# Performance work log

Measured on AMD Instinct MI355X. Metric: run time of the kernel, lower is better.

The kernel has to match this reference:

```python
import jax, jax.numpy as jnp
import numpy as np

B = 128      # args.batch_size
E = 256      # args.num_embed
M = 64       # per-sample positions per embedding channel
S = 3        # number of scales == conv kernel width
C = 5        # args.classes
SCALES = [4, 8, 16]
EPS = 1e-5


def _rnn_last(x, wih, whh, bih, bhh):
    """Elman RNN with input/hidden size 1 over x:(N,T,1); returns last hidden (N,)."""
    xT = jnp.transpose(x[:, :, 0])  # (T, N)
    def step(h, xt):
        h = jnp.tanh(xt * wih + bih + h * whh + bhh)
        return h, None
    h0 = jnp.zeros((x.shape[0],), x.dtype)
    hT, _ = jax.lax.scan(step, h0, xT)
    return hT


def setup_inputs() -> dict:
    key = jax.random.key(0)
    ks = jax.random.split(key, 20)
    N = B * M * E
    inp = {}
    for i, T in enumerate(SCALES):
        inp[f"a{i}"] = jax.random.normal(ks[i], (N, T, 1), dtype=jnp.float32)
    sc = 0.5
    inp["rnn1_wih"] = sc * jax.random.normal(ks[3], (S,), dtype=jnp.float32)
    inp["rnn1_whh"] = sc * jax.random.normal(ks[4], (S,), dtype=jnp.float32)
    inp["rnn1_bih"] = sc * jax.random.normal(ks[5], (S,), dtype=jnp.float32)
    inp["rnn1_bhh"] = sc * jax.random.normal(ks[6], (S,), dtype=jnp.float32)
    inp["conv_w"] = sc * jax.random.normal(ks[7], (S,), dtype=jnp.float32)
    inp["conv_b"] = sc * jax.random.normal(ks[8], (1,), dtype=jnp.float32)
    inp["rnn2_wih"] = sc * jax.random.normal(ks[9], (1,), dtype=jnp.float32)
    inp["rnn2_whh"] = sc * jax.random.normal(ks[10], (1,), dtype=jnp.float32)
    inp["rnn2_bih"] = sc * jax.random.normal(ks[11], (1,), dtype=jnp.float32)
    inp["rnn2_bhh"] = sc * jax.random.normal(ks[12], (1,), dtype=jnp.float32)
    inp["norm_gamma"] = jnp.ones((E,), dtype=jnp.float32)
    inp["norm_beta"] = jnp.zeros((E,), dtype=jnp.float32)
    inp["fnn_w"] = jax.random.normal(ks[13], (C, E), dtype=jnp.float32) / C
    inp["fnn_b"] = jnp.zeros((C,), dtype=jnp.float32)
    return inp


def reference(a0, a1, a2, rnn1_wih, rnn1_whh, rnn1_bih, rnn1_bhh,
              conv_w, conv_b, rnn2_wih, rnn2_whh, rnn2_bih, rnn2_bhh,
              norm_gamma, norm_beta, fnn_w, fnn_b):
    # per-scale scalar RNNs; keep last hidden state, reshape to (B, M, E, 1)
    rst = []
    for i, a in enumerate((a0, a1, a2)):
        h = _rnn_last(a, rnn1_wih[i], rnn1_whh[i], rnn1_bih[i], rnn1_bhh[i])
        rst.append(h.reshape(B, M, E, 1))
    c = jnp.concatenate(rst, axis=-1)          # (B, M, E, S)
    cp = jnp.transpose(c, (0, 2, 1, 3))        # (B, E, M, S)
    # Conv2d(1,1,(1,3)) over (M,S) with S==kernel width -> single output column
    fusion = jnp.einsum('bems,s->bem', cp, conv_w) + conv_b[0]  # (B, E, M)
    # second scalar RNN over the M axis for each (b, e) lane
    seq2 = fusion.reshape(B * E, M, 1)
    h2 = _rnn_last(seq2, rnn2_wih[0], rnn2_whh[0], rnn2_bih[0], rnn2_bhh[0])
    feat = h2.reshape(B, E)
    # BatchNorm1d (training-mode batch statistics, biased variance)
    mean = feat.mean(axis=0)
    var = feat.var(axis=0)
    xn = (feat - mean) / jnp.sqrt(var + EPS) * norm_gamma + norm_beta
    logits = jax.nn.relu(xn) @ fnn_w.T + fnn_b  # (B, C)
    return jax.nn.softmax(logits, axis=1)
```

## Files before the change

kernel.cpp:

```cpp
#include <hip/hip_runtime.h>
#include <math.h>

#define Bb 128
#define Ee 256
#define Mm 64
#define Cc 5
#define NTOT (Bb*Mm*Ee)
#define BE  (Bb*Ee)
#define EPS 1e-5f
#define L2E2 2.8853900817779268f

#if __has_builtin(__builtin_amdgcn_exp2f)
#define EXP2(x) __builtin_amdgcn_exp2f(x)
#else
#define EXP2(x) exp2f(x)
#endif
#define RCP(x) __builtin_amdgcn_rcpf(x)

__device__ __forceinline__ float tanh_step(float x, float w, float b, float u, float h) {
    float t = __builtin_fmaf(x, w, b);
    t = __builtin_fmaf(h, u, t);
    float r = RCP(EXP2(t) + 1.0f);
    return __builtin_fmaf(-2.0f, r, 1.0f);
}

__global__ __launch_bounds__(256) void k_rnn1(
    const float* __restrict__ a0, const float* __restrict__ a1,
    const float* __restrict__ a2,
    const float* __restrict__ wih, const float* __restrict__ whh,
    const float* __restrict__ bih, const float* __restrict__ bhh,
    const float* __restrict__ cw,  const float* __restrict__ cb,
    float* __restrict__ fusion)
{
    int t = blockIdx.x * blockDim.x + threadIdx.x;

    float w0 = wih[0] * L2E2, w1 = wih[1] * L2E2, w2 = wih[2] * L2E2;
    float u0 = whh[0] * L2E2, u1 = whh[1] * L2E2, u2 = whh[2] * L2E2;
    float b0 = (bih[0] + bhh[0]) * L2E2;
    float b1 = (bih[1] + bhh[1]) * L2E2;
    float b2 = (bih[2] + bhh[2]) * L2E2;
    float c0 = cw[0], c1 = cw[1], c2 = cw[2], cbias = cb[0];

    #pragma unroll
    for (int s = 0; s < 2; ++s) {
        int n = t + s * (NTOT / 2);

        float4 x0 = ((const float4*)a0)[n];
        float h0 = tanh_step(x0.x, w0, b0, u0, 0.0f);
        h0 = tanh_step(x0.y, w0, b0, u0, h0);
        h0 = tanh_step(x0.z, w0, b0, u0, h0);
        h0 = tanh_step(x0.w, w0, b0, u0, h0);

        float4 y0 = ((const float4*)a1)[2*n + 0];
        float4 y1 = ((const float4*)a1)[2*n + 1];
        float h1 = tanh_step(y0.x, w1, b1, u1, 0.0f);
        h1 = tanh_step(y0.y, w1, b1, u1, h1);
        h1 = tanh_step(y0.z, w1, b1, u1, h1);
        h1 = tanh_step(y0.w, w1, b1, u1, h1);
        h1 = tanh_step(y1.x, w1, b1, u1, h1);
        h1 = tanh_step(y1.y, w1, b1, u1, h1);
        h1 = tanh_step(y1.z, w1, b1, u1, h1);
        h1 = tanh_step(y1.w, w1, b1, u1, h1);

        float h2 = 0.0f;
        #pragma unroll
        for (int q = 0; q < 4; ++q) {
            float4 z = ((const float4*)a2)[4*n + q];
            h2 = tanh_step(z.x, w2, b2, u2, h2);
            h2 = tanh_step(z.y, w2, b2, u2, h2);
            h2 = tanh_step(z.z, w2, b2, u2, h2);
            h2 = tanh_step(z.w, w2, b2, u2, h2);
        }

        float f = h0 * c0 + h1 * c1 + h2 * c2 + cbias;

        int e = n & (Ee - 1);
        int m = (n >> 8) & (Mm - 1);
        int b = n >> 14;
        fusion[(m << 15) + (b << 8) + e] = f;
    }
}

__global__ __launch_bounds__(256) void k_rnn2(
    const float* __restrict__ fusion,
    const float* __restrict__ w, const float* __restrict__ u,
    const float* __restrict__ bi, const float* __restrict__ bh,
    float* __restrict__ feat)
{
    int j = blockIdx.x * blockDim.x + threadIdx.x;
    float wv = w[0] * L2E2, uv = u[0] * L2E2, bb = (bi[0] + bh[0]) * L2E2;
    float h = 0.0f;
    #pragma unroll 8
    for (int m = 0; m < Mm; ++m) {
        float x = fusion[m * BE + j];
        h = tanh_step(x, wv, bb, uv, h);
    }
    feat[j] = h;
}

__global__ __launch_bounds__(256) void k_stats(
    const float* __restrict__ feat,
    const float* __restrict__ gamma, const float* __restrict__ beta,
    float* __restrict__ scale, float* __restrict__ shift)
{
    int e = threadIdx.x;
    float s = 0.0f, s2 = 0.0f;
    for (int b = 0; b < Bb; ++b) {
        float v = feat[b * Ee + e];
        s  += v;
        s2 += v * v;
    }
    float mean = s * (1.0f / Bb);
    float var  = s2 * (1.0f / Bb) - mean * mean;
    float a = gamma[e] * rsqrtf(var + EPS);
    scale[e] = a;
    shift[e] = beta[e] - mean * a;
}

__global__ __launch_bounds__(256) void k_head(
    const float* __restrict__ feat,
    const float* __restrict__ scale, const float* __restrict__ shift,
    const float* __restrict__ fw, const float* __restrict__ fb,
    float* __restrict__ out)
{
    int b = blockIdx.x;
    int e = threadIdx.x;

    float v = feat[b * Ee + e] * scale[e] + shift[e];
    v = fmaxf(v, 0.0f);

    float p[Cc];
    #pragma unroll
    for (int c = 0; c < Cc; ++c) p[c] = v * fw[c * Ee + e];

    #pragma unroll
    for (int off = 32; off > 0; off >>= 1) {
        #pragma unroll
        for (int c = 0; c < Cc; ++c) p[c] += __shfl_down(p[c], off);
    }

    __shared__ float lds[4][Cc];
    int wave = e >> 6, lane = e & 63;
    if (lane == 0) {
        #pragma unroll
        for (int c = 0; c < Cc; ++c) lds[wave][c] = p[c];
    }
    __syncthreads();

    if (e == 0) {
        float lg[Cc];
        #pragma unroll
        for (int c = 0; c < Cc; ++c)
            lg[c] = lds[0][c] + lds[1][c] + lds[2][c] + lds[3][c] + fb[c];
        float mx = lg[0];
        #pragma unroll
        for (int c = 1; c < Cc; ++c) mx = fmaxf(mx, lg[c]);
        float se = 0.0f;
        #pragma unroll
        for (int c = 0; c < Cc; ++c) { lg[c] = EXP2((lg[c] - mx) * 1.4426950408889634f); se += lg[c]; }
        float inv = RCP(se);
        #pragma unroll
        for (int c = 0; c < Cc; ++c) out[b * Cc + c] = lg[c] * inv;
    }
}

extern "C" void kernel_launch(void* const* d_in, const int* in_sizes, int n_in,
                              void* d_out, int out_size, void* d_ws, size_t ws_size,
                              hipStream_t stream) {
    const float* a0       = (const float*)d_in[0];
    const float* a1       = (const float*)d_in[1];
    const float* a2       = (const float*)d_in[2];
    const float* rnn1_wih = (const float*)d_in[3];
    const float* rnn1_whh = (const float*)d_in[4];
    const float* rnn1_bih = (const float*)d_in[5];
    const float* rnn1_bhh = (const float*)d_in[6];
    const float* conv_w   = (const float*)d_in[7];
    const float* conv_b   = (const float*)d_in[8];
    const float* rnn2_wih = (const float*)d_in[9];
    const float* rnn2_whh = (const float*)d_in[10];
    const float* rnn2_bih = (const float*)d_in[11];
    const float* rnn2_bhh = (const float*)d_in[12];
    const float* gamma    = (const float*)d_in[13];
    const float* beta     = (const float*)d_in[14];
    const float* fnn_w    = (const float*)d_in[15];
    const float* fnn_b    = (const float*)d_in[16];

    float* out = (float*)d_out;

    char* ws = (char*)d_ws;
    float* fusion = (float*)ws;
    float* feat   = (float*)(ws + (size_t)Mm * BE * 4);
    float* scale  = feat + BE;
    float* shift  = scale + Ee;

    k_rnn1<<<NTOT / 2 / 256, 256, 0, stream>>>(a0, a1, a2,
        rnn1_wih, rnn1_whh, rnn1_bih, rnn1_bhh, conv_w, conv_b, fusion);
    k_rnn2<<<BE / 256, 256, 0, stream>>>(fusion,
        rnn2_wih, rnn2_whh, rnn2_bih, rnn2_bhh, feat);
    k_stats<<<1, 256, 0, stream>>>(feat, gamma, beta, scale, shift);
    k_head<<<Bb, 256, 0, stream>>>(feat, scale, shift, fnn_w, fnn_b, out);
}
```

Baseline: 52.08 us.

## Coalesce rnn1 input loads via LDS transpose and fuse BN stats into head

```diff
diff --git a/kernel.cpp b/kernel.cpp
--- a/kernel.cpp
+++ b/kernel.cpp
@@ -32,7 +32,35 @@
     const float* __restrict__ cw,  const float* __restrict__ cb,
     float* __restrict__ fusion)
 {
-    int t = blockIdx.x * blockDim.x + threadIdx.x;
+    __shared__ float a1s[8 * 256];
+    __shared__ float a2s[16 * 257];
+
+    const int t   = threadIdx.x;
+    const int blk = blockIdx.x;
+    const int base = blk << 8;
+
+    float4 x0 = ((const float4*)a0)[base + t];
+
+    #pragma unroll
+    for (int r = 0; r < 2; ++r) {
+        int c = (r << 8) + t;
+        float4 v = ((const float4*)a1)[(size_t)(base << 1) + c];
+        int s = c >> 1, row = (c & 1) << 2;
+        a1s[(row + 0) * 256 + s] = v.x;
+        a1s[(row + 1) * 256 + s] = v.y;
+        a1s[(row + 2) * 256 + s] = v.z;
+        a1s[(row + 3) * 256 + s] = v.w;
+    }
+    #pragma unroll
+    for (int r = 0; r < 4; ++r) {
+        int c = (r << 8) + t;
+        float4 v = ((const float4*)a2)[(size_t)(base << 2) + c];
+        int s = c >> 2, row = (c & 3) << 2;
+        a2s[(row + 0) * 257 + s] = v.x;
+        a2s[(row + 1) * 257 + s] = v.y;
+        a2s[(row + 2) * 257 + s] = v.z;
+        a2s[(row + 3) * 257 + s] = v.w;
+    }
 
     float w0 = wih[0] * L2E2, w1 = wih[1] * L2E2, w2 = wih[2] * L2E2;
     float u0 = whh[0] * L2E2, u1 = whh[1] * L2E2, u2 = whh[2] * L2E2;
@@ -41,44 +69,28 @@
     float b2 = (bih[2] + bhh[2]) * L2E2;
     float c0 = cw[0], c1 = cw[1], c2 = cw[2], cbias = cb[0];
 
-    #pragma unroll
-    for (int s = 0; s < 2; ++s) {
-        int n = t + s * (NTOT / 2);
-
-        float4 x0 = ((const float4*)a0)[n];
-        float h0 = tanh_step(x0.x, w0, b0, u0, 0.0f);
-        h0 = tanh_step(x0.y, w0, b0, u0, h0);
-        h0 = tanh_step(x0.z, w0, b0, u0, h0);
-        h0 = tanh_step(x0.w, w0, b0, u0, h0);
-
-        float4 y0 = ((const float4*)a1)[2*n + 0];
-        float4 y1 = ((const float4*)a1)[2*n + 1];
-        float h1 = tanh_step(y0.x, w1, b1, u1, 0.0f);
-        h1 = tanh_step(y0.y, w1, b1, u1, h1);
-        h1 = tanh_step(y0.z, w1, b1, u1, h1);
-        h1 = tanh_step(y0.w, w1, b1, u1, h1);
-        h1 = tanh_step(y1.x, w1, b1, u1, h1);
-        h1 = tanh_step(y1.y, w1, b1, u1, h1);
-        h1 = tanh_step(y1.z, w1, b1, u1, h1);
-        h1 = tanh_step(y1.w, w1, b1, u1, h1);
-
-        float h2 = 0.0f;
-        #pragma unroll
-        for (int q = 0; q < 4; ++q) {
-            float4 z = ((const float4*)a2)[4*n + q];
-            h2 = tanh_step(z.x, w2, b2, u2, h2);
-            h2 = tanh_step(z.y, w2, b2, u2, h2);
-            h2 = tanh_step(z.z, w2, b2, u2, h2);
-            h2 = tanh_step(z.w, w2, b2, u2, h2);
-        }
-
-        float f = h0 * c0 + h1 * c1 + h2 * c2 + cbias;
-
-        int e = n & (Ee - 1);
-        int m = (n >> 8) & (Mm - 1);
-        int b = n >> 14;
-        fusion[(m << 15) + (b << 8) + e] = f;
-    }
+    __syncthreads();
+
+    float h0 = tanh_step(x0.x, w0, b0, u0, 0.0f);
+    h0 = tanh_step(x0.y, w0, b0, u0, h0);
+    h0 = tanh_step(x0.z, w0, b0, u0, h0);
+    h0 = tanh_step(x0.w, w0, b0, u0, h0);
+
+    float h1 = 0.0f;
+    #pragma unroll
+    for (int k = 0; k < 8; ++k)
+        h1 = tanh_step(a1s[k * 256 + t], w1, b1, u1, h1);
+
+    float h2 = 0.0f;
+    #pragma unroll
+    for (int k = 0; k < 16; ++k)
+        h2 = tanh_step(a2s[k * 257 + t], w2, b2, u2, h2);
+
+    float f = h0 * c0 + h1 * c1 + h2 * c2 + cbias;
+
+    int m = blk & (Mm - 1);
+    int b = blk >> 6;
+    fusion[(m << 15) + (b << 8) + t] = f;
 }
 
 __global__ __launch_bounds__(256) void k_rnn2(
@@ -90,7 +102,7 @@
     int j = blockIdx.x * blockDim.x + threadIdx.x;
     float wv = w[0] * L2E2, uv = u[0] * L2E2, bb = (bi[0] + bh[0]) * L2E2;
     float h = 0.0f;
-    #pragma unroll 8
+    #pragma unroll 16
     for (int m = 0; m < Mm; ++m) {
         float x = fusion[m * BE + j];
         h = tanh_step(x, wv, bb, uv, h);
@@ -98,35 +110,28 @@
     feat[j] = h;
 }
 
-__global__ __launch_bounds__(256) void k_stats(
+__global__ __launch_bounds__(256) void k_head(
     const float* __restrict__ feat,
     const float* __restrict__ gamma, const float* __restrict__ beta,
-    float* __restrict__ scale, float* __restrict__ shift)
-{
-    int e = threadIdx.x;
-    float s = 0.0f, s2 = 0.0f;
-    for (int b = 0; b < Bb; ++b) {
-        float v = feat[b * Ee + e];
-        s  += v;
-        s2 += v * v;
-    }
-    float mean = s * (1.0f / Bb);
-    float var  = s2 * (1.0f / Bb) - mean * mean;
-    float a = gamma[e] * rsqrtf(var + EPS);
-    scale[e] = a;
-    shift[e] = beta[e] - mean * a;
-}
-
-__global__ __launch_bounds__(256) void k_head(
-    const float* __restrict__ feat,
-    const float* __restrict__ scale, const float* __restrict__ shift,
     const float* __restrict__ fw, const float* __restrict__ fb,
     float* __restrict__ out)
 {
     int b = blockIdx.x;
     int e = threadIdx.x;
 
-    float v = feat[b * Ee + e] * scale[e] + shift[e];
+    float s = 0.0f, s2 = 0.0f;
+    #pragma unroll 8
+    for (int bb = 0; bb < Bb; ++bb) {
+        float v = feat[bb * Ee + e];
+        s  += v;
+        s2 += v * v;
+    }
+    float mean = s * (1.0f / Bb);
+    float var  = s2 * (1.0f / Bb) - mean * mean;
+    float a = gamma[e] * rsqrtf(var + EPS);
+    float shift = beta[e] - mean * a;
+
+    float v = feat[b * Ee + e] * a + shift;
     v = fmaxf(v, 0.0f);
 
     float p[Cc];
@@ -190,13 +195,10 @@
     char* ws = (char*)d_ws;
     float* fusion = (float*)ws;
     float* feat   = (float*)(ws + (size_t)Mm * BE * 4);
-    float* scale  = feat + BE;
-    float* shift  = scale + Ee;
-
-    k_rnn1<<<NTOT / 2 / 256, 256, 0, stream>>>(a0, a1, a2,
+
+    k_rnn1<<<NTOT / 256, 256, 0, stream>>>(a0, a1, a2,
         rnn1_wih, rnn1_whh, rnn1_bih, rnn1_bhh, conv_w, conv_b, fusion);
     k_rnn2<<<BE / 256, 256, 0, stream>>>(fusion,
         rnn2_wih, rnn2_whh, rnn2_bih, rnn2_bhh, feat);
-    k_stats<<<1, 256, 0, stream>>>(feat, gamma, beta, scale, shift);
-    k_head<<<Bb, 256, 0, stream>>>(feat, scale, shift, fnn_w, fnn_b, out);
-}
+    k_head<<<Bb, 256, 0, stream>>>(feat, gamma, beta, fnn_w, fnn_b, out);
+}
```

Result: no change. 52.29 us, median of 2 (+0.4%).
